# Kernel tuning notes

Hardware: AMD Instinct MI355X
Metric: run time of the kernel (lower is better)

## Reference

```python
import jax, jax.numpy as jnp
import numpy as np

E = 128          # number of bot groups (envs)
NB = 256         # bots per group
DQ = DK = DV = 256
D = DQ + DK + DV # 768
COM_RANGE = 15.0
KV_NOISE = 0.05
NEG = -1000000.0


def setup_inputs() -> dict:
    key = jax.random.key(0)
    k1, k2, k3, k4 = jax.random.split(key, 4)
    N = E * NB
    qkv = jax.random.normal(k1, (N, D), dtype=jnp.float32)
    # audibility mask: [N_total, n_per_group]; mask[bot_slice] -> [n, n] per group
    mask = jax.random.bernoulli(k2, 0.9, (N, NB))
    # 2D positions in a 30x30 arena so ~half of pairs fall within com_range
    bot_pos = jax.random.uniform(k3, (N, 2), dtype=jnp.float32, minval=0.0, maxval=30.0)
    # kv noise: zero on the q part [:K_DIM], gaussian(std=kv_noise) on k,v part
    noise = jnp.concatenate(
        [jnp.zeros((N, DQ), jnp.float32),
         KV_NOISE * jax.random.normal(k4, (N, DK + DV), dtype=jnp.float32)],
        axis=-1)
    s = jnp.float32(0.0)  # nn.Parameter init
    return {"qkv": qkv, "mask": mask, "bot_pos": bot_pos, "noise": noise, "s": s}


def reference(qkv, mask, bot_pos, noise, s):
    # noise injection on k,v channels (noise is zero on q channels)
    qkv = qkv + noise
    scale_s = jnp.abs(s) + 1.0

    # all bot groups are equal-sized -> batch the per-slice loop as [E, NB, ...]
    qkv_g = qkv.reshape(E, NB, D)
    q = qkv_g[..., :DQ] * scale_s
    k = qkv_g[..., DQ:DQ + DK]
    v = qkv_g[..., DQ + DK:]

    # pairwise-distance range mask per group
    pos = bot_pos.reshape(E, NB, 2)
    bdiff = pos[:, None, :, :] - pos[:, :, None, :]          # [E, NB, NB, 2]
    range_mask = jnp.linalg.norm(bdiff, axis=-1) < COM_RANGE  # [E, NB, NB]

    audible = mask.reshape(E, NB, NB) & range_mask            # [E, NB, NB]

    # SDPA with additive mask (torch adds -1e6 where masked)
    scores = jnp.einsum('eqd,ekd->eqk', q, k) / jnp.sqrt(jnp.float32(DK))
    scores = scores + jnp.where(audible, 0.0, NEG)
    attn = jax.nn.softmax(scores, axis=-1)
    x = jnp.einsum('eqk,ekd->eqd', attn, v)                   # [E, NB, DV]

    # zero out bots that hear nobody
    x = x * audible.any(axis=-1, keepdims=True)
    return x.reshape(E * NB, DV)
```

## Files before the change

### kernel.cpp

```cpp
#include <hip/hip_runtime.h>
#include <hip/hip_bf16.h>
#include <stdint.h>


#define EE   128
#define NBB  256
#define DDIM 768
#define NEGV (-1000000.0f)

typedef __attribute__((ext_vector_type(8))) short short8;
typedef __attribute__((ext_vector_type(4))) float f32x4;

__device__ __forceinline__ unsigned short f2bf(float f){
  union { float f; unsigned u; } v; v.f = f;
  return (unsigned short)((v.u + 0x7FFFu + ((v.u >> 16) & 1u)) >> 16);
}
__device__ __forceinline__ unsigned short cvt1(float f){
  __hip_bfloat16 h = __float2bfloat16(f);
  unsigned short u; __builtin_memcpy(&u, &h, 2); return u;
}
__device__ __forceinline__ unsigned pk2(float lo, float hi){
  return (unsigned)cvt1(lo) | ((unsigned)cvt1(hi) << 16);
}

__device__ __forceinline__ void swap32(unsigned &a, unsigned &b){
#if __has_builtin(__builtin_amdgcn_permlane32_swap)
  auto r = __builtin_amdgcn_permlane32_swap(a, b, false, false);
  a = r[0]; b = r[1];
#else
  const int up = threadIdx.x & 32;
  const unsigned ax = __shfl_xor(a, 32), bx = __shfl_xor(b, 32);
  const unsigned na = up ? bx : a, nb = up ? b : ax;
  a = na; b = nb;
#endif
}
__device__ __forceinline__ void swap16(unsigned &a, unsigned &b){
#if __has_builtin(__builtin_amdgcn_permlane16_swap)
  auto r = __builtin_amdgcn_permlane16_swap(a, b, false, false);
  a = r[0]; b = r[1];
#else
  const int odd = threadIdx.x & 16;
  const unsigned ax = __shfl_xor(a, 16), bx = __shfl_xor(b, 16);
  const unsigned na = odd ? bx : a, nb = odd ? b : ax;
  a = na; b = nb;
#endif
}

__device__ __forceinline__ void gload16(const void* g, void* l){
  __builtin_amdgcn_global_load_lds((const __attribute__((address_space(1))) unsigned*)g,
                                   (__attribute__((address_space(3))) unsigned*)l, 16, 0, 0);
}
__device__ __forceinline__ void gstage(const unsigned short* __restrict__ base,
                                       unsigned short* __restrict__ buf,
                                       int wave, int lane){
  #pragma unroll
  for(int i = 0; i < 8; ++i){
    const int lrow = wave*16 + i*2 + (lane >> 5);
    const int col  = ((lane & 31) * 8) ^ ((lrow & 7) << 3);
    gload16(base + (size_t)lrow * 256 + col, buf + (wave*16 + i*2) * 256);
  }
}

__global__ void k_prep(const float* __restrict__ qkv, const float* __restrict__ noise,
                       unsigned short* __restrict__ Vt, unsigned short* __restrict__ Kb){
  __shared__ unsigned short tile[64 * 66];
  if(blockIdx.x < 2048){
    const int b = blockIdx.x;
    const int e = b >> 4, t4 = b & 15;
    const int k0 = (t4 >> 2) << 6, d0 = (t4 & 3) << 6;
    const int u = threadIdx.x & 15, r = threadIdx.x >> 4;
    #pragma unroll
    for(int i = 0; i < 4; ++i){
      const int kl = r + (i << 4);
      const size_t off = ((size_t)(e*NBB + k0 + kl)) * DDIM + 512 + d0 + (u << 2);
      f32x4 v  = *(const f32x4*)(qkv   + off);
      f32x4 nz = *(const f32x4*)(noise + off);
      const int base = kl * 66 + (u << 2);
      tile[base+0] = f2bf(v[0]+nz[0]); tile[base+1] = f2bf(v[1]+nz[1]);
      tile[base+2] = f2bf(v[2]+nz[2]); tile[base+3] = f2bf(v[3]+nz[3]);
    }
    __syncthreads();
    #pragma unroll
    for(int i = 0; i < 4; ++i){
      const int dl = r + (i << 4);
      unsigned short o0 = tile[(u*4+0)*66 + dl];
      unsigned short o1 = tile[(u*4+1)*66 + dl];
      unsigned short o2 = tile[(u*4+2)*66 + dl];
      unsigned short o3 = tile[(u*4+3)*66 + dl];
      *(ushort4*)(Vt + ((size_t)(e*NBB + d0 + dl)) * NBB + k0 + (u << 2)) =
          make_ushort4(o0, o1, o2, o3);
    }
  } else {
    const int b2 = blockIdx.x - 2048;
    const int n  = b2*8 + (threadIdx.x >> 5);
    const int col = (threadIdx.x & 31) * 8;
    const size_t off = (size_t)n * DDIM + 256 + col;
    f32x4 a0 = *(const f32x4*)(qkv + off),   a1 = *(const f32x4*)(qkv + off + 4);
    f32x4 n0 = *(const f32x4*)(noise + off), n1 = *(const f32x4*)(noise + off + 4);
    short8 o;
    o[0]=f2bf(a0[0]+n0[0]); o[1]=f2bf(a0[1]+n0[1]); o[2]=f2bf(a0[2]+n0[2]); o[3]=f2bf(a0[3]+n0[3]);
    o[4]=f2bf(a1[0]+n1[0]); o[5]=f2bf(a1[1]+n1[1]); o[6]=f2bf(a1[2]+n1[2]); o[7]=f2bf(a1[3]+n1[3]);
    *(short8*)(Kb + (size_t)n * 256 + col) = o;
  }
}

__launch_bounds__(256, 2)
__global__ void k_attn(const float* __restrict__ qkv, const float* __restrict__ sp,
                       const unsigned char* __restrict__ m8, const int* __restrict__ m32,
                       const float* __restrict__ pos,
                       const unsigned short* __restrict__ Vt,
                       const unsigned short* __restrict__ Kb,
                       float* __restrict__ out){
  extern __shared__ unsigned char smem[];
  unsigned short* buf0 = (unsigned short*)smem;
  unsigned short* buf1 = (unsigned short*)(smem + 32768);
  unsigned*       audL = (unsigned*)(smem + 65536);
  float*          posx = (float*)(smem + 67584);
  float*          posy = (float*)(smem + 68608);

  const int bid = blockIdx.x;
  const int e   = ((bid & 7) << 4) + (bid >> 5);
  const int qq  = (bid >> 3) & 3;
  const int tid  = threadIdx.x;
  const int wave = tid >> 6;
  const int lane = tid & 63;
  const int g    = lane >> 4;
  const int u    = lane & 15;
  const int q0   = qq * 64 + wave * 16;
  const size_t ebase = (size_t)e * NBB;

  {
    const float2 p = *(const float2*)(pos + (ebase + tid) * 2);
    posx[tid] = p.x; posy[tid] = p.y;
  }
  const unsigned probe = ((const unsigned*)m32)[tid & 63];
  const int isInt = !__any(probe > 1u);
  __syncthreads();

  gstage(Kb + ebase * 256, buf0, wave, lane);

  #pragma unroll
  for(int h = 0; h < 2; ++h){
    const int w   = tid + h * 256;
    const int row = w >> 3;
    const int j   = w & 7;
    const float qx = posx[qq*64 + row], qy = posy[qq*64 + row];
    const size_t mbase = (ebase + qq*64 + row) * NBB + j * 32;
    unsigned wd = 0u;
    if(isInt){
      #pragma unroll
      for(int i = 0; i < 8; ++i){
        const int4 mv = *(const int4*)(m32 + mbase + i * 4);
        const int mvals[4] = {mv.x, mv.y, mv.z, mv.w};
        #pragma unroll
        for(int jj = 0; jj < 4; ++jj){
          const int kk = i * 4 + jj;
          const int k  = j * 32 + kk;
          const float dx = posx[k] - qx, dy = posy[k] - qy;
          const float d2 = __fadd_rn(__fmul_rn(dx, dx), __fmul_rn(dy, dy));
          if((mvals[jj] != 0) && (sqrtf(d2) < 15.0f)) wd |= 1u << kk;
        }
      }
    } else {
      #pragma unroll
      for(int i = 0; i < 2; ++i){
        const int4 mv = *(const int4*)(m8 + mbase + i * 16);
        const int mvals[4] = {mv.x, mv.y, mv.z, mv.w};
        #pragma unroll
        for(int jj = 0; jj < 4; ++jj)
          #pragma unroll
          for(int b = 0; b < 4; ++b){
            const int kk = i * 16 + jj * 4 + b;
            const int k  = j * 32 + kk;
            const float dx = posx[k] - qx, dy = posy[k] - qy;
            const float d2 = __fadd_rn(__fmul_rn(dx, dx), __fmul_rn(dy, dy));
            if((((unsigned)mvals[jj] >> (8 * b)) & 0xFFu) && (sqrtf(d2) < 15.0f)) wd |= 1u << kk;
          }
      }
    }
    audL[w] = wd;
  }

  const float scale = fabsf(sp[0]) + 1.0f;
  short8 qf[8];
  {
    const float* qrow = qkv + (ebase + q0 + u) * DDIM;
    #pragma unroll
    for(int dk = 0; dk < 8; ++dk){
      f32x4 a = *(const f32x4*)(qrow + dk*32 + g*8);
      f32x4 b = *(const f32x4*)(qrow + dk*32 + g*8 + 4);
      short8 f;
      f[0]=cvt1(a[0]*scale); f[1]=cvt1(a[1]*scale); f[2]=cvt1(a[2]*scale); f[3]=cvt1(a[3]*scale);
      f[4]=cvt1(b[0]*scale); f[5]=cvt1(b[1]*scale); f[6]=cvt1(b[2]*scale); f[7]=cvt1(b[3]*scale);
      qf[dk] = f;
    }
  }

  const f32x4 zero4 = {0.f, 0.f, 0.f, 0.f};
  f32x4 acc[16];
  #pragma unroll
  for(int nt = 0; nt < 16; ++nt) acc[nt] = zero4;

  __syncthreads();

  #pragma unroll
  for(int kq = 0; kq < 4; ++kq){
    unsigned short* cur = (kq & 1) ? buf1 : buf0;
    unsigned short* nxt = (kq & 1) ? buf0 : buf1;
    if(kq < 3) gstage(Kb + (ebase + (size_t)(kq+1) * 64) * 256, nxt, wave, lane);
    else       gstage(Vt + ebase * 256, nxt, wave, lane);
    #pragma unroll
    for(int nth = 0; nth < 4; ++nth){
      const unsigned short* kr = cur + (nth*16 + u) * 256;
      const int sw = (u & 7) << 3;
      #pragma unroll
      for(int dk = 0; dk < 8; ++dk){
        short8 kb = *(const short8*)(kr + ((dk*32 + g*8) ^ sw));
        acc[kq*4 + nth] = __builtin_amdgcn_mfma_f32_16x16x32_bf16(kb, qf[dk], acc[kq*4 + nth], 0, 0, 0);
      }
    }
    if(kq < 3) __syncthreads();
  }

  unsigned wmask[8];
  {
    const unsigned* arow = audL + (wave*16 + u) * 8;
    #pragma unroll
    for(int j = 0; j < 8; ++j) wmask[j] = arow[j];
  }
  const unsigned anyw = wmask[0]|wmask[1]|wmask[2]|wmask[3]|wmask[4]|wmask[5]|wmask[6]|wmask[7];
  const unsigned long long rowsAny = __ballot(anyw != 0u);

  float m0=-3.0e38f, m1=-3.0e38f, m2=-3.0e38f, m3=-3.0e38f;
  #pragma unroll
  for(int nt = 0; nt < 16; ++nt){
    const unsigned wv = wmask[nt >> 1] >> (((nt & 1) << 4) + g*4);
    f32x4 s = acc[nt];
    s[0] = s[0]*0.0625f + ((wv      & 1u) ? 0.0f : NEGV);
    s[1] = s[1]*0.0625f + (((wv>>1) & 1u) ? 0.0f : NEGV);
    s[2] = s[2]*0.0625f + (((wv>>2) & 1u) ? 0.0f : NEGV);
    s[3] = s[3]*0.0625f + (((wv>>3) & 1u) ? 0.0f : NEGV);
    acc[nt] = s;
    m0 = fmaxf(m0, s[0]); m1 = fmaxf(m1, s[1]);
    m2 = fmaxf(m2, s[2]); m3 = fmaxf(m3, s[3]);
  }
  float mx = fmaxf(fmaxf(m0, m1), fmaxf(m2, m3));
  mx = fmaxf(mx, __shfl_xor(mx, 16));
  mx = fmaxf(mx, __shfl_xor(mx, 32));
  float s0=0.f, s1=0.f, s2=0.f, s3=0.f;
  #pragma unroll
  for(int nt = 0; nt < 16; ++nt){
    f32x4 p = acc[nt];
    p[0] = __expf(p[0] - mx); p[1] = __expf(p[1] - mx);
    p[2] = __expf(p[2] - mx); p[3] = __expf(p[3] - mx);
    acc[nt] = p;
    s0 += p[0]; s1 += p[1]; s2 += p[2]; s3 += p[3];
  }
  float ssum = (s0 + s1) + (s2 + s3);
  ssum += __shfl_xor(ssum, 16);
  ssum += __shfl_xor(ssum, 32);
  const float inv = 1.0f / ssum;

  short8 pa[8];
  #pragma unroll
  for(int kt = 0; kt < 8; ++kt){
    unsigned cE = pk2(acc[2*kt][0]*inv,   acc[2*kt][1]*inv);
    unsigned dE = pk2(acc[2*kt][2]*inv,   acc[2*kt][3]*inv);
    unsigned cO = pk2(acc[2*kt+1][0]*inv, acc[2*kt+1][1]*inv);
    unsigned dO = pk2(acc[2*kt+1][2]*inv, acc[2*kt+1][3]*inv);
    swap32(cE, cO); swap16(cE, cO);
    swap32(dE, dO); swap16(dE, dO);
    union { short8 s; unsigned w[4]; } pk;
    pk.w[0] = cE; pk.w[1] = dE; pk.w[2] = cO; pk.w[3] = dO;
    pa[kt] = pk.s;
  }

  __syncthreads();

  #pragma unroll
  for(int dqt = 0; dqt < 4; ++dqt){
    unsigned short* cur = (dqt & 1) ? buf1 : buf0;
    unsigned short* nxt = (dqt & 1) ? buf0 : buf1;
    if(dqt < 3) gstage(Vt + (ebase + (size_t)(dqt+1) * 64) * 256, nxt, wave, lane);
    f32x4 xacc[4];
    #pragma unroll
    for(int dt = 0; dt < 4; ++dt) xacc[dt] = zero4;
    #pragma unroll
    for(int dt = 0; dt < 4; ++dt){
      const unsigned short* vr = cur + (dt*16 + u) * 256;
      const int sw = (u & 7) << 3;
      #pragma unroll
      for(int kt = 0; kt < 8; ++kt){
        short8 bv = *(const short8*)(vr + ((kt*32 + g*8) ^ sw));
        xacc[dt] = __builtin_amdgcn_mfma_f32_16x16x32_bf16(pa[kt], bv, xacc[dt], 0, 0, 0);
      }
    }
    #pragma unroll
    for(int r = 0; r < 4; ++r){
      const float zf = ((rowsAny >> (g*4 + r)) & 1ull) ? 1.0f : 0.0f;
      float* orow = out + (ebase + q0 + g*4 + r) * 256 + dqt*64;
      #pragma unroll
      for(int dt = 0; dt < 4; ++dt)
        orow[dt*16 + u] = xacc[dt][r] * zf;
    }
    if(dqt < 3) __syncthreads();
  }
}

extern "C" void kernel_launch(void* const* d_in, const int* in_sizes, int n_in,
                              void* d_out, int out_size, void* d_ws, size_t ws_size,
                              hipStream_t stream){
  (void)in_sizes; (void)n_in; (void)out_size; (void)ws_size;
  const float* qkv   = (const float*)d_in[0];
  const void*  mask  = d_in[1];
  const float* pos   = (const float*)d_in[2];
  const float* noise = (const float*)d_in[3];
  const float* sp    = (const float*)d_in[4];

  unsigned short* Vt = (unsigned short*)d_ws;
  unsigned short* Kb = (unsigned short*)((unsigned char*)d_ws + 16777216);
  float* outp = (float*)d_out;

  k_prep<<<6144, 256, 0, stream>>>(qkv, noise, Vt, Kb);

  hipFuncSetAttribute((const void*)k_attn, hipFuncAttributeMaxDynamicSharedMemorySize, 69632);
  k_attn<<<512, 256, 69632, stream>>>(qkv, sp,
                                      (const unsigned char*)mask, (const int*)mask,
                                      pos, Vt, Kb, outp);
}
```

Measured before the change: 65.98 us.

## Fuse K noise-add and bf16 conversion into attention kernel; ballot-based mask build

Drops the K-conversion part of the prep kernel. The attention kernel now loads K and noise in fp32 into registers, adds them, converts to bf16 and writes swizzled rows into LDS, prefetching the next 64-row chunk while computing on the current one. This removes the bf16 K round trip through global memory and 4096 prep blocks. In exchange each attention block reads fp32 K four times, since four blocks share an env, and register pressure rises. The audibility mask is also rebuilt so each wave computes one key per lane and packs the bits with __ballot into 64-bit words.

```diff
diff --git a/kernel.cpp b/kernel.cpp
--- a/kernel.cpp
+++ b/kernel.cpp
@@ -61,60 +61,48 @@
   }
 }
 
-__global__ void k_prep(const float* __restrict__ qkv, const float* __restrict__ noise,
-                       unsigned short* __restrict__ Vt, unsigned short* __restrict__ Kb){
+__global__ void k_prep_vt(const float* __restrict__ qkv, const float* __restrict__ noise,
+                          unsigned short* __restrict__ Vt){
   __shared__ unsigned short tile[64 * 66];
-  if(blockIdx.x < 2048){
-    const int b = blockIdx.x;
-    const int e = b >> 4, t4 = b & 15;
-    const int k0 = (t4 >> 2) << 6, d0 = (t4 & 3) << 6;
-    const int u = threadIdx.x & 15, r = threadIdx.x >> 4;
-    #pragma unroll
-    for(int i = 0; i < 4; ++i){
-      const int kl = r + (i << 4);
-      const size_t off = ((size_t)(e*NBB + k0 + kl)) * DDIM + 512 + d0 + (u << 2);
-      f32x4 v  = *(const f32x4*)(qkv   + off);
-      f32x4 nz = *(const f32x4*)(noise + off);
-      const int base = kl * 66 + (u << 2);
-      tile[base+0] = f2bf(v[0]+nz[0]); tile[base+1] = f2bf(v[1]+nz[1]);
-      tile[base+2] = f2bf(v[2]+nz[2]); tile[base+3] = f2bf(v[3]+nz[3]);
-    }
-    __syncthreads();
-    #pragma unroll
-    for(int i = 0; i < 4; ++i){
-      const int dl = r + (i << 4);
-      unsigned short o0 = tile[(u*4+0)*66 + dl];
-      unsigned short o1 = tile[(u*4+1)*66 + dl];
-      unsigned short o2 = tile[(u*4+2)*66 + dl];
-      unsigned short o3 = tile[(u*4+3)*66 + dl];
-      *(ushort4*)(Vt + ((size_t)(e*NBB + d0 + dl)) * NBB + k0 + (u << 2)) =
-          make_ushort4(o0, o1, o2, o3);
-    }
-  } else {
-    const int b2 = blockIdx.x - 2048;
-    const int n  = b2*8 + (threadIdx.x >> 5);
-    const int col = (threadIdx.x & 31) * 8;
-    const size_t off = (size_t)n * DDIM + 256 + col;
-    f32x4 a0 = *(const f32x4*)(qkv + off),   a1 = *(const f32x4*)(qkv + off + 4);
-    f32x4 n0 = *(const f32x4*)(noise + off), n1 = *(const f32x4*)(noise + off + 4);
-    short8 o;
-    o[0]=f2bf(a0[0]+n0[0]); o[1]=f2bf(a0[1]+n0[1]); o[2]=f2bf(a0[2]+n0[2]); o[3]=f2bf(a0[3]+n0[3]);
-    o[4]=f2bf(a1[0]+n1[0]); o[5]=f2bf(a1[1]+n1[1]); o[6]=f2bf(a1[2]+n1[2]); o[7]=f2bf(a1[3]+n1[3]);
-    *(short8*)(Kb + (size_t)n * 256 + col) = o;
+  const int b = blockIdx.x;
+  const int e = b >> 4, t4 = b & 15;
+  const int k0 = (t4 >> 2) << 6, d0 = (t4 & 3) << 6;
+  const int u = threadIdx.x & 15, r = threadIdx.x >> 4;
+  #pragma unroll
+  for(int i = 0; i < 4; ++i){
+    const int kl = r + (i << 4);
+    const size_t off = ((size_t)(e*NBB + k0 + kl)) * DDIM + 512 + d0 + (u << 2);
+    f32x4 v  = *(const f32x4*)(qkv   + off);
+    f32x4 nz = *(const f32x4*)(noise + off);
+    const int base = kl * 66 + (u << 2);
+    tile[base+0] = f2bf(v[0]+nz[0]); tile[base+1] = f2bf(v[1]+nz[1]);
+    tile[base+2] = f2bf(v[2]+nz[2]); tile[base+3] = f2bf(v[3]+nz[3]);
+  }
+  __syncthreads();
+  #pragma unroll
+  for(int i = 0; i < 4; ++i){
+    const int dl = r + (i << 4);
+    unsigned short o0 = tile[(u*4+0)*66 + dl];
+    unsigned short o1 = tile[(u*4+1)*66 + dl];
+    unsigned short o2 = tile[(u*4+2)*66 + dl];
+    unsigned short o3 = tile[(u*4+3)*66 + dl];
+    *(ushort4*)(Vt + ((size_t)(e*NBB + d0 + dl)) * NBB + k0 + (u << 2)) =
+        make_ushort4(o0, o1, o2, o3);
   }
 }
 
 __launch_bounds__(256, 2)
-__global__ void k_attn(const float* __restrict__ qkv, const float* __restrict__ sp,
+__global__ void k_attn(const float* __restrict__ qkv, const float* __restrict__ noise,
+                       const float* __restrict__ sp,
                        const unsigned char* __restrict__ m8, const int* __restrict__ m32,
                        const float* __restrict__ pos,
                        const unsigned short* __restrict__ Vt,
-                       const unsigned short* __restrict__ Kb,
                        float* __restrict__ out){
   extern __shared__ unsigned char smem[];
   unsigned short* buf0 = (unsigned short*)smem;
   unsigned short* buf1 = (unsigned short*)(smem + 32768);
   unsigned*       audL = (unsigned*)(smem + 65536);
+  unsigned long long* audW = (unsigned long long*)(smem + 65536);
   float*          posx = (float*)(smem + 67584);
   float*          posy = (float*)(smem + 68608);
 
@@ -129,6 +117,32 @@
   const int q0   = qq * 64 + wave * 16;
   const size_t ebase = (size_t)e * NBB;
 
+  f32x4 ka[8], kb4[8], na4[8], nb4[8];
+  #define K_ISSUE(kq)                                                          \
+    _Pragma("unroll")                                                          \
+    for(int i = 0; i < 8; ++i){                                                \
+      const int row = wave*16 + i*2 + (lane >> 5);                             \
+      const size_t goff = (ebase + (kq)*64 + row) * DDIM + 256 + (lane & 31)*8;\
+      ka[i]  = *(const f32x4*)(qkv + goff);                                    \
+      kb4[i] = *(const f32x4*)(qkv + goff + 4);                                \
+      na4[i] = *(const f32x4*)(noise + goff);                                  \
+      nb4[i] = *(const f32x4*)(noise + goff + 4);                              \
+    }
+  #define K_WRITE(buf)                                                         \
+    _Pragma("unroll")                                                          \
+    for(int i = 0; i < 8; ++i){                                                \
+      const int row = wave*16 + i*2 + (lane >> 5);                             \
+      short8 o;                                                                \
+      o[0]=cvt1(ka[i][0]+na4[i][0]); o[1]=cvt1(ka[i][1]+na4[i][1]);            \
+      o[2]=cvt1(ka[i][2]+na4[i][2]); o[3]=cvt1(ka[i][3]+na4[i][3]);            \
+      o[4]=cvt1(kb4[i][0]+nb4[i][0]); o[5]=cvt1(kb4[i][1]+nb4[i][1]);          \
+      o[6]=cvt1(kb4[i][2]+nb4[i][2]); o[7]=cvt1(kb4[i][3]+nb4[i][3]);          \
+      const int col = ((lane & 31)*8) ^ ((row & 7) << 3);                      \
+      *(short8*)((buf) + row*256 + col) = o;                                   \
+    }
+
+  K_ISSUE(0);
+
   {
     const float2 p = *(const float2*)(pos + (ebase + tid) * 2);
     posx[tid] = p.x; posy[tid] = p.y;
@@ -137,48 +151,24 @@
   const int isInt = !__any(probe > 1u);
   __syncthreads();
 
-  gstage(Kb + ebase * 256, buf0, wave, lane);
-
-  #pragma unroll
-  for(int h = 0; h < 2; ++h){
-    const int w   = tid + h * 256;
-    const int row = w >> 3;
-    const int j   = w & 7;
-    const float qx = posx[qq*64 + row], qy = posy[qq*64 + row];
-    const size_t mbase = (ebase + qq*64 + row) * NBB + j * 32;
-    unsigned wd = 0u;
-    if(isInt){
+  {
+    const int rowBase = qq*64 + wave*16;
+    #pragma unroll
+    for(int ch = 0; ch < 4; ++ch){
+      const float kx = posx[ch*64 + lane];
+      const float ky = posy[ch*64 + lane];
       #pragma unroll
-      for(int i = 0; i < 8; ++i){
-        const int4 mv = *(const int4*)(m32 + mbase + i * 4);
-        const int mvals[4] = {mv.x, mv.y, mv.z, mv.w};
-        #pragma unroll
-        for(int jj = 0; jj < 4; ++jj){
-          const int kk = i * 4 + jj;
-          const int k  = j * 32 + kk;
-          const float dx = posx[k] - qx, dy = posy[k] - qy;
-          const float d2 = __fadd_rn(__fmul_rn(dx, dx), __fmul_rn(dy, dy));
-          if((mvals[jj] != 0) && (sqrtf(d2) < 15.0f)) wd |= 1u << kk;
-        }
+      for(int rr = 0; rr < 16; ++rr){
+        const float qx = posx[rowBase + rr];
+        const float qy = posy[rowBase + rr];
+        const size_t moff = (ebase + rowBase + rr) * NBB + ch*64 + lane;
+        const int mk = isInt ? m32[moff] : (int)m8[moff];
+        const float dx = kx - qx, dy = ky - qy;
+        const float d2 = __fadd_rn(__fmul_rn(dx, dx), __fmul_rn(dy, dy));
+        const unsigned long long b = __ballot((mk != 0) && (sqrtf(d2) < 15.0f));
+        if(lane == 0) audW[(wave*16 + rr)*4 + ch] = b;
       }
-    } else {
-      #pragma unroll
-      for(int i = 0; i < 2; ++i){
-        const int4 mv = *(const int4*)(m8 + mbase + i * 16);
-        const int mvals[4] = {mv.x, mv.y, mv.z, mv.w};
-        #pragma unroll
-        for(int jj = 0; jj < 4; ++jj)
-          #pragma unroll
-          for(int b = 0; b < 4; ++b){
-            const int kk = i * 16 + jj * 4 + b;
-            const int k  = j * 32 + kk;
-            const float dx = posx[k] - qx, dy = posy[k] - qy;
-            const float d2 = __fadd_rn(__fmul_rn(dx, dx), __fmul_rn(dy, dy));
-            if((((unsigned)mvals[jj] >> (8 * b)) & 0xFFu) && (sqrtf(d2) < 15.0f)) wd |= 1u << kk;
-          }
-      }
-    }
-    audL[w] = wd;
+    }
   }
 
   const float scale = fabsf(sp[0]) + 1.0f;
@@ -201,14 +191,13 @@
   #pragma unroll
   for(int nt = 0; nt < 16; ++nt) acc[nt] = zero4;
 
-  __syncthreads();
-
   #pragma unroll
   for(int kq = 0; kq < 4; ++kq){
     unsigned short* cur = (kq & 1) ? buf1 : buf0;
-    unsigned short* nxt = (kq & 1) ? buf0 : buf1;
-    if(kq < 3) gstage(Kb + (ebase + (size_t)(kq+1) * 64) * 256, nxt, wave, lane);
-    else       gstage(Vt + ebase * 256, nxt, wave, lane);
+    K_WRITE(cur);
+    if(kq < 3) K_ISSUE(kq + 1);
+    __syncthreads();
+    if(kq == 3) gstage(Vt + ebase * 256, buf0, wave, lane);
     #pragma unroll
     for(int nth = 0; nth < 4; ++nth){
       const unsigned short* kr = cur + (nth*16 + u) * 256;
@@ -219,7 +208,6 @@
         acc[kq*4 + nth] = __builtin_amdgcn_mfma_f32_16x16x32_bf16(kb, qf[dk], acc[kq*4 + nth], 0, 0, 0);
       }
     }
-    if(kq < 3) __syncthreads();
   }
 
   unsigned wmask[8];
@@ -318,13 +306,12 @@
   const float* sp    = (const float*)d_in[4];
 
   unsigned short* Vt = (unsigned short*)d_ws;
-  unsigned short* Kb = (unsigned short*)((unsigned char*)d_ws + 16777216);
   float* outp = (float*)d_out;
 
-  k_prep<<<6144, 256, 0, stream>>>(qkv, noise, Vt, Kb);
+  k_prep_vt<<<2048, 256, 0, stream>>>(qkv, noise, Vt);
 
   hipFuncSetAttribute((const void*)k_attn, hipFuncAttributeMaxDynamicSharedMemorySize, 69632);
-  k_attn<<<512, 256, 69632, stream>>>(qkv, sp,
+  k_attn<<<512, 256, 69632, stream>>>(qkv, noise, sp,
                                       (const unsigned char*)mask, (const int*)mask,
-                                      pos, Vt, Kb, outp);
-}
+                                      pos, Vt, outp);
+}
```

Result: slower. 78.81 us (+19.4%).
